# Performance work log

Hardware: AMD Instinct MI355X
Metric: run time of the kernel (lower is better)

The kernel has to match this reference:

```python
import jax, jax.numpy as jnp
import numpy as np


def setup_inputs() -> dict:
    key = jax.random.key(0)
    ks = jax.random.split(key, 8)
    B, N, M = 8, 4096, 4096
    return {
        "R": jax.random.normal(ks[0], (B, 3, 3), dtype=jnp.float32),
        "t": jax.random.normal(ks[1], (B, 3), dtype=jnp.float32),
        "S": jax.random.uniform(ks[2], (B,), dtype=jnp.float32),
        "R_g": jax.random.normal(ks[3], (B, 3, 3), dtype=jnp.float32),
        "t_g": jax.random.normal(ks[4], (B, 3), dtype=jnp.float32),
        "S_g": jax.random.uniform(ks[5], (B,), dtype=jnp.float32),
        "T_X": jax.random.normal(ks[6], (B, N, 3), dtype=jnp.float32),
        "Y": jax.random.normal(ks[7], (B, M, 3), dtype=jnp.float32),
    }


def _chamfer(x, y):
    # x: [B,N,3], y: [B,M,3]. Pairwise Euclidean distances [B,N,M] via the
    x2 = jnp.sum(x * x, axis=-1)                      # [B,N]
    y2 = jnp.sum(y * y, axis=-1)                      # [B,M]
    xy = jnp.einsum('bnd,bmd->bnm', x, y)             # [B,N,M]
    d2 = x2[:, :, None] + y2[:, None, :] - 2.0 * xy
    dist = jnp.sqrt(jnp.maximum(d2, 0.0))             # [B,N,M]
    min_x_to_y = jnp.min(dist, axis=2)                # [B,N]
    min_y_to_x = jnp.min(dist, axis=1)                # [B,M]
    per_batch = jnp.mean(min_x_to_y, axis=1) + jnp.mean(min_y_to_x, axis=1)
    return jnp.mean(per_batch)


def _registration(R, t, S, R_g, t_g, S_g):
    eye = jnp.eye(3, dtype=R.dtype)
    diff = jnp.einsum('bji,bjk->bik', R_g, R) - eye   # R_g^T @ R - I, [B,3,3]
    L_R = jnp.sum(diff * diff, axis=(1, 2))           # squared Frobenius norm
    L_t = jnp.sum((t_g - t) ** 2, axis=1)
    L_S = (S_g - S) ** 2
    return jnp.mean(L_R + L_t + L_S)


def reference(R, t, S, R_g, t_g, S_g, T_X, Y):
    L_R = _registration(R, t, S, R_g, t_g, S_g)
    L_CD = _chamfer(T_X, Y)
    return (L_R + L_CD, L_R, L_CD)
```

## Files before the change

### kernel.cpp

```cpp
#include <hip/hip_runtime.h>
#include <hip/hip_bf16.h>

constexpr int B_ = 8;
constexpr int N_ = 4096;
constexpr int M_ = 4096;
constexpr int TPB = 256;
constexpr int QPT = 4;
constexpr int QPB = TPB * QPT;
constexpr int QBLKS = N_ / QPB;
constexpr int SPLIT = 16;
constexpr int CHUNK = M_ / SPLIT;
constexpr int NQ = 2 * B_ * N_;

__global__ __launch_bounds__(TPB) void chamfer_pass1(
    const float* __restrict__ X, const float* __restrict__ Yp,
    float* __restrict__ part)
{
    __shared__ float4 sdb[CHUNK];

    int bid = blockIdx.x;
    const int dir   = bid & 1;             bid >>= 1;
    const int chunk = bid & (SPLIT - 1);   bid >>= 4;
    const int qblk  = bid & (QBLKS - 1);   bid >>= 2;
    const int b     = bid;

    const float* q  = dir ? Yp : X;
    const float* db = dir ? X  : Yp;

    const int t = threadIdx.x;

    {
        const float* src = db + (size_t)(b * M_ + chunk * CHUNK + t) * 3;
        float a0 = src[0], a1 = src[1], a2 = src[2];
        sdb[t] = make_float4(-2.0f * a0, -2.0f * a1, -2.0f * a2,
                             a0 * a0 + a1 * a1 + a2 * a2);
    }

    float qx[QPT], qy[QPT], qz[QPT], qn[QPT];
    const int qbase = b * N_ + qblk * QPB;
    #pragma unroll
    for (int k = 0; k < QPT; ++k) {
        const float* qp = q + (size_t)(qbase + k * TPB + t) * 3;
        qx[k] = qp[0]; qy[k] = qp[1]; qz[k] = qp[2];
        qn[k] = qx[k] * qx[k] + qy[k] * qy[k] + qz[k] * qz[k];
    }
    __syncthreads();

    const float BIG = 3.0e38f;
    float mA[QPT], mB[QPT];
    #pragma unroll
    for (int k = 0; k < QPT; ++k) { mA[k] = BIG; mB[k] = BIG; }

    #pragma unroll 2
    for (int j = 0; j < CHUNK; j += 4) {
        float4 p0 = sdb[j + 0];
        float4 p1 = sdb[j + 1];
        float4 p2 = sdb[j + 2];
        float4 p3 = sdb[j + 3];
        #pragma unroll
        for (int k = 0; k < QPT; ++k) {
            mA[k] = fminf(mA[k], fmaf(qx[k], p0.x, fmaf(qy[k], p0.y, fmaf(qz[k], p0.z, p0.w))));
            mB[k] = fminf(mB[k], fmaf(qx[k], p1.x, fmaf(qy[k], p1.y, fmaf(qz[k], p1.z, p1.w))));
            mA[k] = fminf(mA[k], fmaf(qx[k], p2.x, fmaf(qy[k], p2.y, fmaf(qz[k], p2.z, p2.w))));
            mB[k] = fminf(mB[k], fmaf(qx[k], p3.x, fmaf(qy[k], p3.y, fmaf(qz[k], p3.z, p3.w))));
        }
    }

    const int wbase = chunk * NQ + dir * (B_ * N_) + qbase;
    #pragma unroll
    for (int k = 0; k < QPT; ++k) {
        float d2 = fmaxf(fminf(mA[k], mB[k]) + qn[k], 0.0f);
        part[wbase + k * TPB + t] = d2;
    }
}

__global__ __launch_bounds__(TPB) void min_sqrt_sum(
    const float* __restrict__ part, float* __restrict__ bsum)
{
    __shared__ float wsum[TPB / 64];
    const int qid = blockIdx.x * TPB + threadIdx.x;

    float m = part[qid];
    #pragma unroll
    for (int c = 1; c < SPLIT; ++c) m = fminf(m, part[c * NQ + qid]);
    float d = sqrtf(m);

    #pragma unroll
    for (int off = 32; off > 0; off >>= 1) d += __shfl_down(d, off, 64);
    if ((threadIdx.x & 63) == 0) wsum[threadIdx.x >> 6] = d;
    __syncthreads();
    if (threadIdx.x == 0)
        bsum[blockIdx.x] = wsum[0] + wsum[1] + wsum[2] + wsum[3];
}

__global__ __launch_bounds__(TPB) void final_kernel(
    const float* __restrict__ bsum,
    const float* __restrict__ R,  const float* __restrict__ t,
    const float* __restrict__ S,  const float* __restrict__ Rg,
    const float* __restrict__ tg, const float* __restrict__ Sg,
    float* __restrict__ out)
{
    __shared__ float wsum[4];
    __shared__ float sreg[8];
    const int tid = threadIdx.x;

    float s = bsum[tid];
    #pragma unroll
    for (int off = 32; off > 0; off >>= 1) s += __shfl_down(s, off, 64);
    if ((tid & 63) == 0) wsum[tid >> 6] = s;

    if (tid < 8) {
        const float* Rb  = R  + tid * 9;
        const float* Rgb = Rg + tid * 9;
        float acc = 0.0f;
        #pragma unroll
        for (int i = 0; i < 3; ++i) {
            #pragma unroll
            for (int k = 0; k < 3; ++k) {
                float v = 0.0f;
                #pragma unroll
                for (int j = 0; j < 3; ++j)
                    v = fmaf(Rgb[j * 3 + i], Rb[j * 3 + k], v);
                if (i == k) v -= 1.0f;
                acc = fmaf(v, v, acc);
            }
        }
        #pragma unroll
        for (int d = 0; d < 3; ++d) {
            float dv = tg[tid * 3 + d] - t[tid * 3 + d];
            acc = fmaf(dv, dv, acc);
        }
        float dS = Sg[tid] - S[tid];
        acc = fmaf(dS, dS, acc);
        sreg[tid] = acc;
    }
    __syncthreads();

    if (tid == 0) {
        float tot = wsum[0] + wsum[1] + wsum[2] + wsum[3];
        float L_CD = tot / (float)(B_ * N_);
        float rs = 0.0f;
        #pragma unroll
        for (int bb = 0; bb < 8; ++bb) rs += sreg[bb];
        float L_R = rs / (float)B_;
        out[0] = L_R + L_CD;
        out[1] = L_R;
        out[2] = L_CD;
    }
}

extern "C" void kernel_launch(void* const* d_in, const int* in_sizes, int n_in,
                              void* d_out, int out_size, void* d_ws, size_t ws_size,
                              hipStream_t stream) {
    const float* R  = (const float*)d_in[0];
    const float* t  = (const float*)d_in[1];
    const float* S  = (const float*)d_in[2];
    const float* Rg = (const float*)d_in[3];
    const float* tg = (const float*)d_in[4];
    const float* Sg = (const float*)d_in[5];
    const float* X  = (const float*)d_in[6];
    const float* Yp = (const float*)d_in[7];
    float* out = (float*)d_out;

    float* part = (float*)d_ws;
    float* bsum = part + (size_t)SPLIT * NQ;

    chamfer_pass1<<<2 * B_ * QBLKS * SPLIT, TPB, 0, stream>>>(X, Yp, part);
    min_sqrt_sum<<<NQ / TPB, TPB, 0, stream>>>(part, bsum);
    final_kernel<<<1, TPB, 0, stream>>>(bsum, R, t, S, Rg, tg, Sg, out);
}
```

Before: 92.08 us.

## Use packed FP32 FMA in chamfer inner loop and fuse final reduction via atomics

The inner distance loop now uses v_pk_fma_f32 on pairs of database points, stored interleaved in shared memory so each packed load holds the same coordinate for two points, with four independent min accumulators per query. The min/sqrt/sum kernel and the final scalar kernel are merged into one launch that accumulates per-block sums into the output with atomicAdd after a memset. This aims to halve the FMA instruction count in the hot loop and remove one kernel launch. The trade-offs are 256 floating-point atomics on the same few addresses, which make the summation order nondeterministic, and an extra memset on the stream.

Result: slower. 95.78 us (+4.0%).

```diff
diff --git a/kernel.cpp b/kernel.cpp
--- a/kernel.cpp
+++ b/kernel.cpp
@@ -10,13 +10,22 @@
 constexpr int QBLKS = N_ / QPB;
 constexpr int SPLIT = 16;
 constexpr int CHUNK = M_ / SPLIT;
+constexpr int NPAIR = CHUNK / 2;
 constexpr int NQ = 2 * B_ * N_;
+
+typedef float v2f __attribute__((ext_vector_type(2)));
+
+static __device__ __forceinline__ v2f pk_fma(v2f a, v2f b, v2f c) {
+    v2f d;
+    asm("v_pk_fma_f32 %0, %1, %2, %3" : "=v"(d) : "v"(a), "v"(b), "v"(c));
+    return d;
+}
 
 __global__ __launch_bounds__(TPB) void chamfer_pass1(
     const float* __restrict__ X, const float* __restrict__ Yp,
     float* __restrict__ part)
 {
-    __shared__ float4 sdb[CHUNK];
+    __shared__ float sdb8[NPAIR * 8];
 
     int bid = blockIdx.x;
     const int dir   = bid & 1;             bid >>= 1;
@@ -32,53 +41,69 @@
     {
         const float* src = db + (size_t)(b * M_ + chunk * CHUNK + t) * 3;
         float a0 = src[0], a1 = src[1], a2 = src[2];
-        sdb[t] = make_float4(-2.0f * a0, -2.0f * a1, -2.0f * a2,
-                             a0 * a0 + a1 * a1 + a2 * a2);
+        const int base = (t >> 1) * 8 + (t & 1);
+        sdb8[base + 0] = -2.0f * a0;
+        sdb8[base + 2] = -2.0f * a1;
+        sdb8[base + 4] = -2.0f * a2;
+        sdb8[base + 6] = a0 * a0 + a1 * a1 + a2 * a2;
     }
 
-    float qx[QPT], qy[QPT], qz[QPT], qn[QPT];
+    v2f qxx[QPT], qyy[QPT], qzz[QPT];
+    float qn[QPT];
     const int qbase = b * N_ + qblk * QPB;
     #pragma unroll
     for (int k = 0; k < QPT; ++k) {
         const float* qp = q + (size_t)(qbase + k * TPB + t) * 3;
-        qx[k] = qp[0]; qy[k] = qp[1]; qz[k] = qp[2];
-        qn[k] = qx[k] * qx[k] + qy[k] * qy[k] + qz[k] * qz[k];
+        float x = qp[0], y = qp[1], z = qp[2];
+        qxx[k] = (v2f){x, x};
+        qyy[k] = (v2f){y, y};
+        qzz[k] = (v2f){z, z};
+        qn[k]  = x * x + y * y + z * z;
     }
     __syncthreads();
 
+    const v2f* s2 = (const v2f*)sdb8;
     const float BIG = 3.0e38f;
-    float mA[QPT], mB[QPT];
+    float mA[QPT], mB[QPT], mC[QPT], mD[QPT];
     #pragma unroll
-    for (int k = 0; k < QPT; ++k) { mA[k] = BIG; mB[k] = BIG; }
+    for (int k = 0; k < QPT; ++k) { mA[k] = BIG; mB[k] = BIG; mC[k] = BIG; mD[k] = BIG; }
 
     #pragma unroll 2
-    for (int j = 0; j < CHUNK; j += 4) {
-        float4 p0 = sdb[j + 0];
-        float4 p1 = sdb[j + 1];
-        float4 p2 = sdb[j + 2];
-        float4 p3 = sdb[j + 3];
+    for (int j = 0; j < NPAIR; j += 2) {
+        v2f xx0 = s2[4 * j + 0], yy0 = s2[4 * j + 1];
+        v2f zz0 = s2[4 * j + 2], ww0 = s2[4 * j + 3];
+        v2f xx1 = s2[4 * j + 4], yy1 = s2[4 * j + 5];
+        v2f zz1 = s2[4 * j + 6], ww1 = s2[4 * j + 7];
         #pragma unroll
         for (int k = 0; k < QPT; ++k) {
-            mA[k] = fminf(mA[k], fmaf(qx[k], p0.x, fmaf(qy[k], p0.y, fmaf(qz[k], p0.z, p0.w))));
-            mB[k] = fminf(mB[k], fmaf(qx[k], p1.x, fmaf(qy[k], p1.y, fmaf(qz[k], p1.z, p1.w))));
-            mA[k] = fminf(mA[k], fmaf(qx[k], p2.x, fmaf(qy[k], p2.y, fmaf(qz[k], p2.z, p2.w))));
-            mB[k] = fminf(mB[k], fmaf(qx[k], p3.x, fmaf(qy[k], p3.y, fmaf(qz[k], p3.z, p3.w))));
+            v2f d0 = pk_fma(qxx[k], xx0, pk_fma(qyy[k], yy0, pk_fma(qzz[k], zz0, ww0)));
+            v2f d1 = pk_fma(qxx[k], xx1, pk_fma(qyy[k], yy1, pk_fma(qzz[k], zz1, ww1)));
+            mA[k] = fminf(mA[k], d0.x);
+            mB[k] = fminf(mB[k], d0.y);
+            mC[k] = fminf(mC[k], d1.x);
+            mD[k] = fminf(mD[k], d1.y);
         }
     }
 
     const int wbase = chunk * NQ + dir * (B_ * N_) + qbase;
     #pragma unroll
     for (int k = 0; k < QPT; ++k) {
-        float d2 = fmaxf(fminf(mA[k], mB[k]) + qn[k], 0.0f);
-        part[wbase + k * TPB + t] = d2;
+        float m = fminf(fminf(mA[k], mB[k]), fminf(mC[k], mD[k]));
+        part[wbase + k * TPB + t] = fmaxf(m + qn[k], 0.0f);
     }
 }
 
-__global__ __launch_bounds__(TPB) void min_sqrt_sum(
-    const float* __restrict__ part, float* __restrict__ bsum)
+__global__ __launch_bounds__(TPB) void finalize_fused(
+    const float* __restrict__ part,
+    const float* __restrict__ R,  const float* __restrict__ t,
+    const float* __restrict__ S,  const float* __restrict__ Rg,
+    const float* __restrict__ tg, const float* __restrict__ Sg,
+    float* __restrict__ out)
 {
     __shared__ float wsum[TPB / 64];
-    const int qid = blockIdx.x * TPB + threadIdx.x;
+    __shared__ float sreg[8];
+    const int tid = threadIdx.x;
+    const int qid = blockIdx.x * TPB + tid;
 
     float m = part[qid];
     #pragma unroll
@@ -87,29 +112,9 @@
 
     #pragma unroll
     for (int off = 32; off > 0; off >>= 1) d += __shfl_down(d, off, 64);
-    if ((threadIdx.x & 63) == 0) wsum[threadIdx.x >> 6] = d;
-    __syncthreads();
-    if (threadIdx.x == 0)
-        bsum[blockIdx.x] = wsum[0] + wsum[1] + wsum[2] + wsum[3];
-}
+    if ((tid & 63) == 0) wsum[tid >> 6] = d;
 
-__global__ __launch_bounds__(TPB) void final_kernel(
-    const float* __restrict__ bsum,
-    const float* __restrict__ R,  const float* __restrict__ t,
-    const float* __restrict__ S,  const float* __restrict__ Rg,
-    const float* __restrict__ tg, const float* __restrict__ Sg,
-    float* __restrict__ out)
-{
-    __shared__ float wsum[4];
-    __shared__ float sreg[8];
-    const int tid = threadIdx.x;
-
-    float s = bsum[tid];
-    #pragma unroll
-    for (int off = 32; off > 0; off >>= 1) s += __shfl_down(s, off, 64);
-    if ((tid & 63) == 0) wsum[tid >> 6] = s;
-
-    if (tid < 8) {
+    if (blockIdx.x == 0 && tid < 8) {
         const float* Rb  = R  + tid * 9;
         const float* Rgb = Rg + tid * 9;
         float acc = 0.0f;
@@ -126,8 +131,8 @@
             }
         }
         #pragma unroll
-        for (int d = 0; d < 3; ++d) {
-            float dv = tg[tid * 3 + d] - t[tid * 3 + d];
+        for (int dd = 0; dd < 3; ++dd) {
+            float dv = tg[tid * 3 + dd] - t[tid * 3 + dd];
             acc = fmaf(dv, dv, acc);
         }
         float dS = Sg[tid] - S[tid];
@@ -137,15 +142,17 @@
     __syncthreads();
 
     if (tid == 0) {
-        float tot = wsum[0] + wsum[1] + wsum[2] + wsum[3];
-        float L_CD = tot / (float)(B_ * N_);
-        float rs = 0.0f;
-        #pragma unroll
-        for (int bb = 0; bb < 8; ++bb) rs += sreg[bb];
-        float L_R = rs / (float)B_;
-        out[0] = L_R + L_CD;
-        out[1] = L_R;
-        out[2] = L_CD;
+        float bs = (wsum[0] + wsum[1] + wsum[2] + wsum[3]) * (1.0f / (B_ * N_));
+        atomicAdd(&out[0], bs);
+        atomicAdd(&out[2], bs);
+        if (blockIdx.x == 0) {
+            float rs = 0.0f;
+            #pragma unroll
+            for (int bb = 0; bb < 8; ++bb) rs += sreg[bb];
+            float L_R = rs * (1.0f / B_);
+            atomicAdd(&out[0], L_R);
+            atomicAdd(&out[1], L_R);
+        }
     }
 }
 
@@ -163,9 +170,8 @@
     float* out = (float*)d_out;
 
     float* part = (float*)d_ws;
-    float* bsum = part + (size_t)SPLIT * NQ;
 
+    hipMemsetAsync(out, 0, 3 * sizeof(float), stream);
     chamfer_pass1<<<2 * B_ * QBLKS * SPLIT, TPB, 0, stream>>>(X, Yp, part);
-    min_sqrt_sum<<<NQ / TPB, TPB, 0, stream>>>(part, bsum);
-    final_kernel<<<1, TPB, 0, stream>>>(bsum, R, t, S, Rg, tg, Sg, out);
+    finalize_fused<<<NQ / TPB, TPB, 0, stream>>>(part, R, t, S, Rg, tg, Sg, out);
 }
```
